# Optimization experiments

Hardware: AMD Instinct MI355X
Metric: run time of the kernel (lower is better)

## Reference

```python
import jax, jax.numpy as jnp
import numpy as np

N = 100000   # nodes
E = 1600000  # edges (avg degree 16)
DIN, DH, DOUT = 128, 128, 64


def setup_inputs() -> dict:
    key = jax.random.key(0)
    ks = jax.random.split(key, 10)
    x = jax.random.normal(ks[0], (N, DIN), dtype=jnp.float32)
    edge_index = jax.random.randint(ks[1], (2, E), 0, N, dtype=jnp.int32)

    def kaiming(k, fan_out, fan_in):
        # kaiming_uniform_ with nonlinearity='relu': bound = sqrt(6/fan_in)
        bound = np.sqrt(6.0 / fan_in)
        return jax.random.uniform(k, (fan_out, fan_in), jnp.float32, -bound, bound)

    W1 = kaiming(ks[2], DH, DIN)
    W2 = kaiming(ks[3], DH, DH)
    W3 = kaiming(ks[4], DH, DH)
    W4 = kaiming(ks[5], DOUT, DH)
    b1 = jnp.zeros((DH,), jnp.float32)
    b2 = jnp.zeros((DH,), jnp.float32)
    b3 = jnp.zeros((DH,), jnp.float32)
    b4 = jnp.zeros((DOUT,), jnp.float32)
    return {"x": x, "edge_index": edge_index,
            "W1": W1, "b1": b1, "W2": W2, "b2": b2,
            "W3": W3, "b3": b3, "W4": W4, "b4": b4}


def reference(x, edge_index, W1, b1, W2, b2, W3, b3, W4, b4):
    n = x.shape[0]
    src, dst = edge_index[0], edge_index[1]
    # gcn_norm with add_self_loops=False: deg = in-degree at dst (unit weights)
    deg = jax.ops.segment_sum(jnp.ones(src.shape[0], x.dtype), dst, num_segments=n)
    deg_inv_sqrt = jnp.where(deg > 0, jax.lax.rsqrt(jnp.maximum(deg, 1.0)) * jnp.sqrt(jnp.maximum(deg, 1.0)) / jnp.maximum(deg, 1.0) * jnp.sqrt(jnp.maximum(deg, 1.0)), 0.0)
    deg_inv_sqrt = jnp.where(deg > 0, 1.0 / jnp.sqrt(jnp.maximum(deg, 1.0)), 0.0)
    norm = deg_inv_sqrt[src] * deg_inv_sqrt[dst]  # [E]

    def gcn_layer(h, W, b):
        h = h @ W.T                                # [n, out] dense transform
        msg = h[src] * norm[:, None]               # gather + scale  [E, out]
        out = jax.ops.segment_sum(msg, dst, num_segments=n)  # scatter-add
        return out + b

    h = jax.nn.relu(gcn_layer(x, W1, b1))
    h = jax.nn.relu(gcn_layer(h, W2, b2))
    h = jax.nn.relu(gcn_layer(h, W3, b3))
    return gcn_layer(h, W4, b4)
```

## Files before the change

### kernel.cpp

```cpp
#include <hip/hip_runtime.h>
#include <hip/hip_bf16.h>

#define CAP 64
#define BCAP 250000

typedef __attribute__((ext_vector_type(8))) short bf16x8;
typedef __attribute__((ext_vector_type(4))) float f32x4;
typedef _Float16 f16;
typedef __attribute__((ext_vector_type(2))) _Float16 f16x2;

__device__ __forceinline__ ushort f2bf(float f) {
    uint u = __float_as_uint(f);
    u = u + 0x7FFF + ((u >> 16) & 1);
    return (ushort)(u >> 16);
}
__device__ __forceinline__ float bf2f(ushort b) { return __uint_as_float(((uint)b) << 16); }

__device__ __forceinline__ int bkt(int d, int r) {
    int b = 0;
    if (d >= 4 * r) b = 4;
    if (d >= (b + 2) * r) b += 2;
    if (d >= (b + 1) * r) b += 1;
    return b;
}

__global__ __launch_bounds__(256) void route_kernel(const int* __restrict__ src,
                                                    const int* __restrict__ dst,
                                                    int E, int N,
                                                    uint* __restrict__ buf,
                                                    int* __restrict__ gcur) {
    __shared__ int lcnt[8], lbase[8];
    if (threadIdx.x < 8) lcnt[threadIdx.x] = 0;
    __syncthreads();
    const int r = (N + 7) >> 3;
    const int e = (blockIdx.x * 256 + threadIdx.x) * 4;
    int bb[4]; uint pk[4]; int ne = 0;
    if (e + 4 <= E) {
        int4 d4 = *(const int4*)(dst + e);
        int4 s4 = *(const int4*)(src + e);
        int ds[4] = {d4.x, d4.y, d4.z, d4.w};
        int ss[4] = {s4.x, s4.y, s4.z, s4.w};
#pragma unroll
        for (int k = 0; k < 4; ++k) {
            int d = ds[k];
            int b = bkt(d, r);
            bb[k] = b;
            pk[k] = ((uint)ss[k] << 14) | (uint)(d - b * r);
            atomicAdd(&lcnt[b], 1);
        }
        ne = 4;
    } else {
        for (int t = e; t < E; ++t) {
            int d = dst[t];
            int b = bkt(d, r);
            bb[ne] = b;
            pk[ne] = ((uint)src[t] << 14) | (uint)(d - b * r);
            atomicAdd(&lcnt[b], 1);
            ++ne;
        }
    }
    __syncthreads();
    if (threadIdx.x < 8) {
        lbase[threadIdx.x] = atomicAdd(&gcur[threadIdx.x], lcnt[threadIdx.x]);
        lcnt[threadIdx.x] = 0;
    }
    __syncthreads();
    for (int k = 0; k < ne; ++k) {
        int idx = lbase[bb[k]] + atomicAdd(&lcnt[bb[k]], 1);
        if (idx < BCAP) buf[(size_t)bb[k] * BCAP + idx] = pk[k];
    }
}

__global__ __launch_bounds__(256) void fill_kernel(const uint* __restrict__ buf,
                                                   const int* __restrict__ gcur,
                                                   int* __restrict__ fil,
                                                   int* __restrict__ csr, int N) {
    const int xg = blockIdx.x & 7;
    const int gidx = blockIdx.x >> 3;
    const int ngrp = gridDim.x >> 3;
    const int r = (N + 7) >> 3;
    const int lo = xg * r;
    int cnt = gcur[xg];
    if (cnt > BCAP) cnt = BCAP;
    const uint* b = buf + (size_t)xg * BCAP;
    for (int i = gidx * 256 + threadIdx.x; i < cnt; i += ngrp * 256) {
        uint pk = b[i];
        int d = lo + (int)(pk & 0x3FFFu);
        int s = (int)(pk >> 14);
        int p = atomicAdd(&fil[d], 1);
        if (p < CAP) csr[(size_t)d * CAP + p] = s;
    }
}

__global__ void prep_kernel(const float* __restrict__ W1, const float* __restrict__ W2,
                            const float* __restrict__ W3, const float* __restrict__ W4,
                            ushort* __restrict__ hilo,
                            const int* __restrict__ cnt, float* __restrict__ dis, int N) {
    int blk = blockIdx.x;
    if (blk < 224) {
        int i = blk * 256 + threadIdx.x;
        const float* W;
        ushort* hi;
        int off;
        if (i < 16384)      { W = W1; hi = hilo;          off = i; }
        else if (i < 32768) { W = W2; hi = hilo + 32768;  off = i - 16384; }
        else if (i < 49152) { W = W3; hi = hilo + 65536;  off = i - 32768; }
        else                { W = W4; hi = hilo + 98304;  off = i - 49152; }
        float w = W[off];
        ushort h = f2bf(w);
        int span = (i < 49152) ? 16384 : 8192;
        hi[off] = h;
        hi[off + span] = f2bf(w - bf2f(h));
    } else {
        int i = (blk - 224) * 256 + threadIdx.x;
        if (i < N) {
            int c = cnt[i];
            dis[i] = (c > 0) ? rsqrtf((float)c) : 0.0f;
        }
    }
}

template <int COLS>
__global__ __launch_bounds__(256) void mfma_gemm_kernel(const float* __restrict__ F,
                                                        const ushort* __restrict__ Whi,
                                                        const ushort* __restrict__ Wlo,
                                                        const float* __restrict__ dis,
                                                        f16* __restrict__ G, int N) {
    constexpr int CT = COLS / 16;
    const int wave = threadIdx.x >> 6;
    const int lane = threadIdx.x & 63;
    const int lr = lane & 15;
    const int kg = lane >> 4;

    const int rowBase = blockIdx.x * 128 + wave * 32;

    f32x4 acc[2][CT];
#pragma unroll
    for (int rt = 0; rt < 2; ++rt)
#pragma unroll
        for (int c = 0; c < CT; ++c) acc[rt][c] = (f32x4){0.f, 0.f, 0.f, 0.f};

#pragma unroll
    for (int kt = 0; kt < 4; ++kt) {
        bf16x8 Ah[2], Al[2];
#pragma unroll
        for (int rt = 0; rt < 2; ++rt) {
            int row = rowBase + rt * 16 + lr;
            row = row < N ? row : N - 1;
            const float* p = F + (size_t)row * 128 + kt * 32 + kg * 8;
            float4 v0 = *(const float4*)p;
            float4 v1 = *(const float4*)(p + 4);
            float f[8] = {v0.x, v0.y, v0.z, v0.w, v1.x, v1.y, v1.z, v1.w};
            bf16x8 h, l;
#pragma unroll
            for (int j = 0; j < 8; ++j) {
                ushort hb = f2bf(f[j]);
                h[j] = (short)hb;
                l[j] = (short)f2bf(f[j] - bf2f(hb));
            }
            Ah[rt] = h;
            Al[rt] = l;
        }
#pragma unroll
        for (int c = 0; c < CT; ++c) {
            const size_t wo = (size_t)(c * 16 + lr) * 128 + kt * 32 + kg * 8;
            bf16x8 Bh = *(const bf16x8*)(Whi + wo);
            bf16x8 Bl = *(const bf16x8*)(Wlo + wo);
#pragma unroll
            for (int rt = 0; rt < 2; ++rt) {
                acc[rt][c] = __builtin_amdgcn_mfma_f32_16x16x32_bf16(Al[rt], Bh, acc[rt][c], 0, 0, 0);
                acc[rt][c] = __builtin_amdgcn_mfma_f32_16x16x32_bf16(Ah[rt], Bl, acc[rt][c], 0, 0, 0);
                acc[rt][c] = __builtin_amdgcn_mfma_f32_16x16x32_bf16(Ah[rt], Bh, acc[rt][c], 0, 0, 0);
            }
        }
    }

#pragma unroll
    for (int rt = 0; rt < 2; ++rt) {
#pragma unroll
        for (int j = 0; j < 4; ++j) {
            int row = rowBase + rt * 16 + kg * 4 + j;
            if (row < N) {
                float d = dis[row];
#pragma unroll
                for (int c = 0; c < CT; ++c)
                    G[(size_t)row * COLS + c * 16 + lr] = (f16)(acc[rt][c][j] * d);
            }
        }
    }
}

template <int WIDTH, bool DO_RELU>
__global__ __launch_bounds__(256) void agg_kernel(const f16* __restrict__ g,
                                                  const int* __restrict__ csr,
                                                  const int* __restrict__ cnt,
                                                  const float* __restrict__ dis,
                                                  const float* __restrict__ bias,
                                                  float* __restrict__ out, int N) {
    constexpr int VPL = WIDTH / 64;
    int node = blockIdx.x * 4 + (threadIdx.x >> 6);
    if (node >= N) return;
    int lane = threadIdx.x & 63;

    int c = cnt[node];
    if (c > CAP) c = CAP;
    const int* lst = csr + (size_t)node * CAP;
    float acc0 = 0.f, acc1 = 0.f;

    int j = 0;
    for (; j + 8 <= c; j += 8) {
        int4 sA = *(const int4*)(lst + j);
        int4 sB = *(const int4*)(lst + j + 4);
        if (VPL == 2) {
            f16x2 t0 = *(const f16x2*)(g + (size_t)sA.x * WIDTH + lane * 2);
            f16x2 t1 = *(const f16x2*)(g + (size_t)sA.y * WIDTH + lane * 2);
            f16x2 t2 = *(const f16x2*)(g + (size_t)sA.z * WIDTH + lane * 2);
            f16x2 t3 = *(const f16x2*)(g + (size_t)sA.w * WIDTH + lane * 2);
            f16x2 t4 = *(const f16x2*)(g + (size_t)sB.x * WIDTH + lane * 2);
            f16x2 t5 = *(const f16x2*)(g + (size_t)sB.y * WIDTH + lane * 2);
            f16x2 t6 = *(const f16x2*)(g + (size_t)sB.z * WIDTH + lane * 2);
            f16x2 t7 = *(const f16x2*)(g + (size_t)sB.w * WIDTH + lane * 2);
            acc0 += (((float)t0[0] + (float)t1[0]) + ((float)t2[0] + (float)t3[0])) +
                    (((float)t4[0] + (float)t5[0]) + ((float)t6[0] + (float)t7[0]));
            acc1 += (((float)t0[1] + (float)t1[1]) + ((float)t2[1] + (float)t3[1])) +
                    (((float)t4[1] + (float)t5[1]) + ((float)t6[1] + (float)t7[1]));
        } else {
            float u0 = (float)g[(size_t)sA.x * WIDTH + lane];
            float u1 = (float)g[(size_t)sA.y * WIDTH + lane];
            float u2 = (float)g[(size_t)sA.z * WIDTH + lane];
            float u3 = (float)g[(size_t)sA.w * WIDTH + lane];
            float u4 = (float)g[(size_t)sB.x * WIDTH + lane];
            float u5 = (float)g[(size_t)sB.y * WIDTH + lane];
            float u6 = (float)g[(size_t)sB.z * WIDTH + lane];
            float u7 = (float)g[(size_t)sB.w * WIDTH + lane];
            acc0 += ((u0 + u1) + (u2 + u3)) + ((u4 + u5) + (u6 + u7));
        }
    }
    for (; j + 4 <= c; j += 4) {
        int4 sA = *(const int4*)(lst + j);
        if (VPL == 2) {
            f16x2 t0 = *(const f16x2*)(g + (size_t)sA.x * WIDTH + lane * 2);
            f16x2 t1 = *(const f16x2*)(g + (size_t)sA.y * WIDTH + lane * 2);
            f16x2 t2 = *(const f16x2*)(g + (size_t)sA.z * WIDTH + lane * 2);
            f16x2 t3 = *(const f16x2*)(g + (size_t)sA.w * WIDTH + lane * 2);
            acc0 += ((float)t0[0] + (float)t1[0]) + ((float)t2[0] + (float)t3[0]);
            acc1 += ((float)t0[1] + (float)t1[1]) + ((float)t2[1] + (float)t3[1]);
        } else {
            float u0 = (float)g[(size_t)sA.x * WIDTH + lane];
            float u1 = (float)g[(size_t)sA.y * WIDTH + lane];
            float u2 = (float)g[(size_t)sA.z * WIDTH + lane];
            float u3 = (float)g[(size_t)sA.w * WIDTH + lane];
            acc0 += (u0 + u1) + (u2 + u3);
        }
    }
    for (; j < c; ++j) {
        int s = lst[j];
        if (VPL == 2) {
            f16x2 t = *(const f16x2*)(g + (size_t)s * WIDTH + lane * 2);
            acc0 += (float)t[0];
            acc1 += (float)t[1];
        } else {
            acc0 += (float)g[(size_t)s * WIDTH + lane];
        }
    }

    float d = dis[node];
    if (VPL == 2) {
        float v0 = fmaf(d, acc0, bias[lane * 2 + 0]);
        float v1 = fmaf(d, acc1, bias[lane * 2 + 1]);
        if (DO_RELU) { v0 = fmaxf(v0, 0.f); v1 = fmaxf(v1, 0.f); }
        float2 o = make_float2(v0, v1);
        *(float2*)(out + (size_t)node * WIDTH + lane * 2) = o;
    } else {
        float v0 = fmaf(d, acc0, bias[lane]);
        if (DO_RELU) v0 = fmaxf(v0, 0.f);
        out[(size_t)node * WIDTH + lane] = v0;
    }
}

extern "C" void kernel_launch(void* const* d_in, const int* in_sizes, int n_in,
                              void* d_out, int out_size, void* d_ws, size_t ws_size,
                              hipStream_t stream) {
    const float* x  = (const float*)d_in[0];
    const int*   ei = (const int*)d_in[1];
    const float* W1 = (const float*)d_in[2];
    const float* b1 = (const float*)d_in[3];
    const float* W2 = (const float*)d_in[4];
    const float* b2 = (const float*)d_in[5];
    const float* W3 = (const float*)d_in[6];
    const float* b3 = (const float*)d_in[7];
    const float* W4 = (const float*)d_in[8];
    const float* b4 = (const float*)d_in[9];

    const int N = in_sizes[0] / 128;
    const int E = in_sizes[1] / 2;
    const int* src = ei;
    const int* dst = ei + E;

    char* w = (char*)d_ws;
    float* F   = (float*)w; w += (size_t)N * 128 * 4;
    f16*   G   = (f16*)w;   w += (size_t)N * 128 * 4;
    int*   csr = (int*)w;   w += (size_t)N * CAP * 4;
    float* dis = (float*)w; w += (size_t)N * 4;
    int*   fil = (int*)w;   w += (size_t)(N + 8) * 4;
    int*   gcur = fil + N;
    ushort* Whl = (ushort*)w; w += (16384 * 6 + 8192 * 2) * 2;
    ushort* Whi1 = Whl;          ushort* Wlo1 = Whl + 16384;
    ushort* Whi2 = Whl + 32768;  ushort* Wlo2 = Whl + 49152;
    ushort* Whi3 = Whl + 65536;  ushort* Wlo3 = Whl + 81920;
    ushort* Whi4 = Whl + 98304;  ushort* Wlo4 = Whl + 106496;
    uint* buf = (uint*)G;

    float* out = (float*)d_out;

    hipMemsetAsync(fil, 0, (size_t)(N + 8) * sizeof(int), stream);

    const int nq = (E + 3) / 4;
    route_kernel<<<(nq + 255) / 256, 256, 0, stream>>>(src, dst, E, N, buf, gcur);
    fill_kernel<<<2048, 256, 0, stream>>>(buf, gcur, fil, csr, N);
    prep_kernel<<<224 + (N + 255) / 256, 256, 0, stream>>>(W1, W2, W3, W4, Whl, fil, dis, N);

    const int gemm_grid = (N + 127) / 128;
    const int agg_grid  = (N + 3) / 4;

    mfma_gemm_kernel<128><<<gemm_grid, 256, 0, stream>>>(x, Whi1, Wlo1, dis, G, N);
    agg_kernel<128, true><<<agg_grid, 256, 0, stream>>>(G, csr, fil, dis, b1, F, N);
    mfma_gemm_kernel<128><<<gemm_grid, 256, 0, stream>>>(F, Whi2, Wlo2, dis, G, N);
    agg_kernel<128, true><<<agg_grid, 256, 0, stream>>>(G, csr, fil, dis, b2, F, N);
    mfma_gemm_kernel<128><<<gemm_grid, 256, 0, stream>>>(F, Whi3, Wlo3, dis, G, N);
    agg_kernel<128, true><<<agg_grid, 256, 0, stream>>>(G, csr, fil, dis, b3, F, N);
    mfma_gemm_kernel<64><<<gemm_grid, 256, 0, stream>>>(F, Whi4, Wlo4, dis, G, N);
    agg_kernel<64, false><<<agg_grid, 256, 0, stream>>>(G, csr, fil, dis, b4, out, N);
}
```

Baseline: 604.8 us.

## Add two-level edge bucketing with LDS fill, fp16 hidden activations, XCD-aware agg order

Replaces the global-atomic CSR fill with a second routing pass into 512-destination sub-buckets, then fills each sub-bucket's CSR rows using LDS atomics and writes the degree counts directly. Intermediate activations between layers are now stored as fp16 instead of fp32, which halves their write and read traffic. The aggregation block index is remapped so each of the 8 block groups handles a contiguous range of nodes, aiming for better L2 locality per XCD. This adds a kernel launch and lowers activation precision, and the fixed sub-bucket capacity could overflow on skewed degree distributions.

```diff
diff --git a/kernel.cpp b/kernel.cpp
--- a/kernel.cpp
+++ b/kernel.cpp
@@ -3,11 +3,13 @@
 
 #define CAP 64
 #define BCAP 250000
+#define SBCAP 12288
 
 typedef __attribute__((ext_vector_type(8))) short bf16x8;
 typedef __attribute__((ext_vector_type(4))) float f32x4;
 typedef _Float16 f16;
 typedef __attribute__((ext_vector_type(2))) _Float16 f16x2;
+typedef __attribute__((ext_vector_type(8))) _Float16 f16x8;
 
 __device__ __forceinline__ ushort f2bf(float f) {
     uint u = __float_as_uint(f);
@@ -28,7 +30,7 @@
                                                     const int* __restrict__ dst,
                                                     int E, int N,
                                                     uint* __restrict__ buf,
-                                                    int* __restrict__ gcur) {
+                                                    int* __restrict__ gcur8) {
     __shared__ int lcnt[8], lbase[8];
     if (threadIdx.x < 8) lcnt[threadIdx.x] = 0;
     __syncthreads();
@@ -42,26 +44,24 @@
         int ss[4] = {s4.x, s4.y, s4.z, s4.w};
 #pragma unroll
         for (int k = 0; k < 4; ++k) {
-            int d = ds[k];
-            int b = bkt(d, r);
+            int b = bkt(ds[k], r);
             bb[k] = b;
-            pk[k] = ((uint)ss[k] << 14) | (uint)(d - b * r);
+            pk[k] = ((uint)ss[k] << 14) | (uint)(ds[k] - b * r);
             atomicAdd(&lcnt[b], 1);
         }
         ne = 4;
     } else {
         for (int t = e; t < E; ++t) {
-            int d = dst[t];
-            int b = bkt(d, r);
+            int b = bkt(dst[t], r);
             bb[ne] = b;
-            pk[ne] = ((uint)src[t] << 14) | (uint)(d - b * r);
+            pk[ne] = ((uint)src[t] << 14) | (uint)(dst[t] - b * r);
             atomicAdd(&lcnt[b], 1);
             ++ne;
         }
     }
     __syncthreads();
     if (threadIdx.x < 8) {
-        lbase[threadIdx.x] = atomicAdd(&gcur[threadIdx.x], lcnt[threadIdx.x]);
+        lbase[threadIdx.x] = atomicAdd(&gcur8[threadIdx.x], lcnt[threadIdx.x]);
         lcnt[threadIdx.x] = 0;
     }
     __syncthreads();
@@ -71,24 +71,73 @@
     }
 }
 
-__global__ __launch_bounds__(256) void fill_kernel(const uint* __restrict__ buf,
-                                                   const int* __restrict__ gcur,
-                                                   int* __restrict__ fil,
-                                                   int* __restrict__ csr, int N) {
+__global__ __launch_bounds__(256) void reroute_kernel(const uint* __restrict__ buf,
+                                                      const int* __restrict__ gcur8,
+                                                      uint* __restrict__ buf2,
+                                                      int* __restrict__ gcur2, int NSUB) {
+    __shared__ int lcnt[32], lbase[32];
     const int xg = blockIdx.x & 7;
     const int gidx = blockIdx.x >> 3;
-    const int ngrp = gridDim.x >> 3;
-    const int r = (N + 7) >> 3;
-    const int lo = xg * r;
-    int cnt = gcur[xg];
+    if (threadIdx.x < NSUB) lcnt[threadIdx.x] = 0;
+    __syncthreads();
+    int cnt = gcur8[xg];
     if (cnt > BCAP) cnt = BCAP;
     const uint* b = buf + (size_t)xg * BCAP;
-    for (int i = gidx * 256 + threadIdx.x; i < cnt; i += ngrp * 256) {
-        uint pk = b[i];
-        int d = lo + (int)(pk & 0x3FFFu);
+    const int e0 = (gidx * 256 + threadIdx.x) * 4;
+    uint pk[4]; int sb_[4]; int ne = 0;
+    if (e0 + 4 <= cnt) {
+        uint4 v = *(const uint4*)(b + e0);
+        pk[0] = v.x; pk[1] = v.y; pk[2] = v.z; pk[3] = v.w; ne = 4;
+    } else {
+        for (int t = e0; t < cnt; ++t) pk[ne++] = b[t];
+    }
+    for (int k = 0; k < ne; ++k) {
+        int sub = (int)(pk[k] & 0x3FFFu) >> 9;
+        sb_[k] = sub;
+        atomicAdd(&lcnt[sub], 1);
+    }
+    __syncthreads();
+    if (threadIdx.x < NSUB) {
+        lbase[threadIdx.x] = atomicAdd(&gcur2[xg * NSUB + threadIdx.x], lcnt[threadIdx.x]);
+        lcnt[threadIdx.x] = 0;
+    }
+    __syncthreads();
+    for (int k = 0; k < ne; ++k) {
+        int idx = lbase[sb_[k]] + atomicAdd(&lcnt[sb_[k]], 1);
+        if (idx < SBCAP) buf2[(size_t)(xg * NSUB + sb_[k]) * SBCAP + idx] = pk[k];
+    }
+}
+
+__global__ __launch_bounds__(256) void fillsort_kernel(const uint* __restrict__ buf2,
+                                                       const int* __restrict__ gcur2,
+                                                       int* __restrict__ fil,
+                                                       int* __restrict__ csr, int N, int NSUB) {
+    __shared__ uint stage[SBCAP];
+    __shared__ int lcnt[512];
+    const int xg = blockIdx.x & 7;
+    const int sub = blockIdx.x >> 3;
+    const int sb = xg * NSUB + sub;
+    const int r = (N + 7) >> 3;
+    const int lo_dl = sub << 9;
+    const int ndst = min(512, r - lo_dl);
+    if (ndst <= 0) return;
+    int cnt = gcur2[sb];
+    if (cnt > SBCAP) cnt = SBCAP;
+    for (int i = threadIdx.x; i < cnt; i += 256) stage[i] = buf2[(size_t)sb * SBCAP + i];
+    for (int i = threadIdx.x; i < ndst; i += 256) lcnt[i] = 0;
+    __syncthreads();
+    const int lo_d = xg * r + lo_dl;
+    for (int i = threadIdx.x; i < cnt; i += 256) {
+        uint pk = stage[i];
+        int dll = (int)(pk & 0x3FFFu) - lo_dl;
         int s = (int)(pk >> 14);
-        int p = atomicAdd(&fil[d], 1);
-        if (p < CAP) csr[(size_t)d * CAP + p] = s;
+        int p = atomicAdd(&lcnt[dll], 1);
+        if (p < CAP) csr[(size_t)(lo_d + dll) * CAP + p] = s;
+    }
+    __syncthreads();
+    for (int i = threadIdx.x; i < ndst; i += 256) {
+        int d = lo_d + i;
+        if (d < N) fil[d] = lcnt[i];
     }
 }
 
@@ -120,8 +169,8 @@
     }
 }
 
-template <int COLS>
-__global__ __launch_bounds__(256) void mfma_gemm_kernel(const float* __restrict__ F,
+template <int COLS, typename FT>
+__global__ __launch_bounds__(256) void mfma_gemm_kernel(const FT* __restrict__ F,
                                                         const ushort* __restrict__ Whi,
                                                         const ushort* __restrict__ Wlo,
                                                         const float* __restrict__ dis,
@@ -147,10 +196,18 @@
         for (int rt = 0; rt < 2; ++rt) {
             int row = rowBase + rt * 16 + lr;
             row = row < N ? row : N - 1;
-            const float* p = F + (size_t)row * 128 + kt * 32 + kg * 8;
-            float4 v0 = *(const float4*)p;
-            float4 v1 = *(const float4*)(p + 4);
-            float f[8] = {v0.x, v0.y, v0.z, v0.w, v1.x, v1.y, v1.z, v1.w};
+            const FT* p = F + (size_t)row * 128 + kt * 32 + kg * 8;
+            float f[8];
+            if constexpr (sizeof(FT) == 4) {
+                float4 v0 = *(const float4*)p;
+                float4 v1 = *(const float4*)(p + 4);
+                f[0] = v0.x; f[1] = v0.y; f[2] = v0.z; f[3] = v0.w;
+                f[4] = v1.x; f[5] = v1.y; f[6] = v1.z; f[7] = v1.w;
+            } else {
+                f16x8 v = *(const f16x8*)p;
+#pragma unroll
+                for (int j = 0; j < 8; ++j) f[j] = (float)v[j];
+            }
             bf16x8 h, l;
 #pragma unroll
             for (int j = 0; j < 8; ++j) {
@@ -190,15 +247,17 @@
     }
 }
 
-template <int WIDTH, bool DO_RELU>
+template <int WIDTH, bool DO_RELU, typename OT>
 __global__ __launch_bounds__(256) void agg_kernel(const f16* __restrict__ g,
                                                   const int* __restrict__ csr,
                                                   const int* __restrict__ cnt,
                                                   const float* __restrict__ dis,
                                                   const float* __restrict__ bias,
-                                                  float* __restrict__ out, int N) {
+                                                  OT* __restrict__ out, int N) {
     constexpr int VPL = WIDTH / 64;
-    int node = blockIdx.x * 4 + (threadIdx.x >> 6);
+    const int nb8 = gridDim.x >> 3;
+    const int vblk = (blockIdx.x & 7) * nb8 + (blockIdx.x >> 3);
+    int node = vblk * 4 + (threadIdx.x >> 6);
     if (node >= N) return;
     int lane = threadIdx.x & 63;
 
@@ -269,12 +328,17 @@
         float v0 = fmaf(d, acc0, bias[lane * 2 + 0]);
         float v1 = fmaf(d, acc1, bias[lane * 2 + 1]);
         if (DO_RELU) { v0 = fmaxf(v0, 0.f); v1 = fmaxf(v1, 0.f); }
-        float2 o = make_float2(v0, v1);
-        *(float2*)(out + (size_t)node * WIDTH + lane * 2) = o;
+        if constexpr (sizeof(OT) == 2) {
+            f16x2 o = {(f16)v0, (f16)v1};
+            *(f16x2*)(out + (size_t)node * WIDTH + lane * 2) = o;
+        } else {
+            float2 o = make_float2(v0, v1);
+            *(float2*)(out + (size_t)node * WIDTH + lane * 2) = o;
+        }
     } else {
         float v0 = fmaf(d, acc0, bias[lane]);
         if (DO_RELU) v0 = fmaxf(v0, 0.f);
-        out[(size_t)node * WIDTH + lane] = v0;
+        out[(size_t)node * WIDTH + lane] = (OT)v0;
     }
 }
 
@@ -296,39 +360,45 @@
     const int E = in_sizes[1] / 2;
     const int* src = ei;
     const int* dst = ei + E;
+    const int r = (N + 7) >> 3;
+    const int NSUB = (r + 511) >> 9;
 
     char* w = (char*)d_ws;
-    float* F   = (float*)w; w += (size_t)N * 128 * 4;
-    f16*   G   = (f16*)w;   w += (size_t)N * 128 * 4;
+    f16*   F   = (f16*)w;   w += (size_t)N * 128 * 2;
+    f16*   G   = (f16*)w;   w += (size_t)N * 128 * 2;
     int*   csr = (int*)w;   w += (size_t)N * CAP * 4;
     float* dis = (float*)w; w += (size_t)N * 4;
-    int*   fil = (int*)w;   w += (size_t)(N + 8) * 4;
-    int*   gcur = fil + N;
+    int*   fil = (int*)w;   w += (size_t)N * 4;
+    int*   gcur8 = (int*)w; w += 8 * 4;
+    int*   gcur2 = (int*)w; w += (size_t)8 * NSUB * 4;
     ushort* Whl = (ushort*)w; w += (16384 * 6 + 8192 * 2) * 2;
     ushort* Whi1 = Whl;          ushort* Wlo1 = Whl + 16384;
     ushort* Whi2 = Whl + 32768;  ushort* Wlo2 = Whl + 49152;
     ushort* Whi3 = Whl + 65536;  ushort* Wlo3 = Whl + 81920;
     ushort* Whi4 = Whl + 98304;  ushort* Wlo4 = Whl + 106496;
-    uint* buf = (uint*)G;
+    uint* buf  = (uint*)G;
+    uint* buf2 = (uint*)G + (size_t)8 * BCAP;
 
     float* out = (float*)d_out;
 
-    hipMemsetAsync(fil, 0, (size_t)(N + 8) * sizeof(int), stream);
+    hipMemsetAsync(fil, 0, ((size_t)N + 8 + (size_t)8 * NSUB) * sizeof(int), stream);
 
     const int nq = (E + 3) / 4;
-    route_kernel<<<(nq + 255) / 256, 256, 0, stream>>>(src, dst, E, N, buf, gcur);
-    fill_kernel<<<2048, 256, 0, stream>>>(buf, gcur, fil, csr, N);
+    route_kernel<<<(nq + 255) / 256, 256, 0, stream>>>(src, dst, E, N, buf, gcur8);
+    const int ngrp = ((E / 8) + 1023) / 1024 + 4;
+    reroute_kernel<<<8 * ngrp, 256, 0, stream>>>(buf, gcur8, buf2, gcur2, NSUB);
+    fillsort_kernel<<<8 * NSUB, 256, 0, stream>>>(buf2, gcur2, fil, csr, N, NSUB);
     prep_kernel<<<224 + (N + 255) / 256, 256, 0, stream>>>(W1, W2, W3, W4, Whl, fil, dis, N);
 
     const int gemm_grid = (N + 127) / 128;
-    const int agg_grid  = (N + 3) / 4;
-
-    mfma_gemm_kernel<128><<<gemm_grid, 256, 0, stream>>>(x, Whi1, Wlo1, dis, G, N);
-    agg_kernel<128, true><<<agg_grid, 256, 0, stream>>>(G, csr, fil, dis, b1, F, N);
-    mfma_gemm_kernel<128><<<gemm_grid, 256, 0, stream>>>(F, Whi2, Wlo2, dis, G, N);
-    agg_kernel<128, true><<<agg_grid, 256, 0, stream>>>(G, csr, fil, dis, b2, F, N);
-    mfma_gemm_kernel<128><<<gemm_grid, 256, 0, stream>>>(F, Whi3, Wlo3, dis, G, N);
-    agg_kernel<128, true><<<agg_grid, 256, 0, stream>>>(G, csr, fil, dis, b3, F, N);
-    mfma_gemm_kernel<64><<<gemm_grid, 256, 0, stream>>>(F, Whi4, Wlo4, dis, G, N);
-    agg_kernel<64, false><<<agg_grid, 256, 0, stream>>>(G, csr, fil, dis, b4, out, N);
-}
+    const int agg_grid  = (((N + 3) / 4 + 7) / 8) * 8;
+
+    mfma_gemm_kernel<128, float><<<gemm_grid, 256, 0, stream>>>(x, Whi1, Wlo1, dis, G, N);
+    agg_kernel<128, true, f16><<<agg_grid, 256, 0, stream>>>(G, csr, fil, dis, b1, F, N);
+    mfma_gemm_kernel<128, f16><<<gemm_grid, 256, 0, stream>>>(F, Whi2, Wlo2, dis, G, N);
+    agg_kernel<128, true, f16><<<agg_grid, 256, 0, stream>>>(G, csr, fil, dis, b2, F, N);
+    mfma_gemm_kernel<128, f16><<<gemm_grid, 256, 0, stream>>>(F, Whi3, Wlo3, dis, G, N);
+    agg_kernel<128, true, f16><<<agg_grid, 256, 0, stream>>>(G, csr, fil, dis, b3, F, N);
+    mfma_gemm_kernel<64, f16><<<gemm_grid, 256, 0, stream>>>(F, Whi4, Wlo4, dis, G, N);
+    agg_kernel<64, false, float><<<agg_grid, 256, 0, stream>>>(G, csr, fil, dis, b4, out, N);
+}
```

Measured after the change: 543.1 us. -10.2%, faster.
